# Kernel optimization log

Hardware: AMD Instinct MI355X
Metric: run time of the kernel (lower is better)

## Reference

```python
import jax, jax.numpy as jnp
import numpy as np
import math

B, C, H, W = 2, 256, 64, 64
E = 256           # embed_dim
AE = 64           # angle embed dim = embed_dim // 4
NH = 3            # num angle hypotheses
HEADS = 8
HALF = AE // 2    # 32 sin/cos frequencies

# 3x3 kernel tap grid (dy, dx), row-major, matching torchvision DeformConv2d tap order
KY = jnp.array([-1,-1,-1, 0,0,0, 1,1,1], jnp.float32)
KX = jnp.array([-1, 0, 1,-1,0,1,-1,0,1], jnp.float32)
# assumed angle hypothesis deltas around the predicted angle
HYPO_DELTAS = (-math.pi/12, 0.0, math.pi/12)


def conv2d(x, w, b, pad):
    y = jax.lax.conv_general_dilated(x, w, (1, 1), [(pad, pad), (pad, pad)],
                                     dimension_numbers=('NCHW', 'OIHW', 'NCHW'))
    return y + b[None, :, None, None]


def gen_offsets(angles):
    """Rotate the base 3x3 kernel taps by the per-pixel angle; offset = rotated - base.
    angles: (B, H*W, 1) -> offsets (B, 18, H, W), (dy,dx) interleaved per tap."""
    a = angles.reshape(-1, H, W)
    c = jnp.cos(a)[..., None]           # (B,H,W,1)
    s = jnp.sin(a)[..., None]
    ry = KX * s + KY * c                # rotated y of each tap, (B,H,W,9)
    rx = KX * c - KY * s                # rotated x
    off = jnp.stack([ry - KY, rx - KX], axis=-1)   # (B,H,W,9,2)
    return off.reshape(-1, H, W, 18).transpose(0, 3, 1, 2)


def deform_conv(x, offsets, w, b):
    """DeformConv2d k=3, stride=1, pad=1, dilation=1, zero padding outside.
    x (B,C,H,W), offsets (B,18,H,W), w (O,C,3,3)."""
    off = offsets.reshape(x.shape[0], 9, 2, H, W)
    oy = off[:, :, 0].transpose(0, 2, 3, 1)          # (B,H,W,9)
    ox = off[:, :, 1].transpose(0, 2, 3, 1)
    hh = jnp.arange(H, dtype=jnp.float32)[None, :, None, None]
    ww = jnp.arange(W, dtype=jnp.float32)[None, None, :, None]
    py = hh + KY + oy                                # sample y, (B,H,W,9)
    px = ww + KX + ox
    y0 = jnp.floor(py)
    x0 = jnp.floor(px)
    wy = (py - y0)[:, None]                          # (B,1,H,W,9)
    wx = (px - x0)[:, None]

    def gather(yi, xi):
        valid = (yi >= 0) & (yi <= H - 1) & (xi >= 0) & (xi <= W - 1)
        yc = jnp.clip(yi, 0, H - 1).astype(jnp.int32)
        xc = jnp.clip(xi, 0, W - 1).astype(jnp.int32)
        g = jax.vmap(lambda img, yy, xx: img[:, yy, xx])(x, yc, xc)  # (B,C,H,W,9)
        return g * valid[:, None].astype(x.dtype)

    samp = (gather(y0, x0) * (1 - wy) * (1 - wx)
            + gather(y0, x0 + 1) * (1 - wy) * wx
            + gather(y0 + 1, x0) * wy * (1 - wx)
            + gather(y0 + 1, x0 + 1) * wy * wx)      # (B,C,H,W,9)
    w9 = w.reshape(w.shape[0], w.shape[1], 9)
    return jnp.einsum('bchwk,ock->bohw', samp, w9) + b[None, :, None, None]


def angle_encode(angles, freq_mult, w1, b1, ln_g, ln_b, w2, b2):
    an = (angles / (math.pi / 2))[..., 0]                       # (B,HW) le90 norm
    dim_t = jnp.arange(HALF, dtype=jnp.float32) / HALF * math.pi
    ae = an[..., None] * (freq_mult * dim_t)                    # (B,HW,HALF)
    emb = jnp.concatenate([jnp.sin(ae), jnp.cos(ae)], axis=-1)  # (B,HW,AE)
    h = emb @ w1.T + b1
    mu = h.mean(-1, keepdims=True)
    var = h.var(-1, keepdims=True)
    h = (h - mu) * jax.lax.rsqrt(var + 1e-5) * ln_g + ln_b
    return jax.nn.relu(h) @ w2.T + b2


def mha(q, kv, in_w, in_b, out_w, out_b):
    # q (L,1,E), kv (L,NH,E); torch nn.MultiheadAttention math
    wq, wk, wv = jnp.split(in_w, 3, axis=0)
    bq, bk, bv = jnp.split(in_b, 3)
    hd = E // HEADS
    Q = (q @ wq.T + bq).reshape(-1, 1, HEADS, hd).transpose(0, 2, 1, 3)
    K = (kv @ wk.T + bk).reshape(-1, NH, HEADS, hd).transpose(0, 2, 1, 3)
    V = (kv @ wv.T + bv).reshape(-1, NH, HEADS, hd).transpose(0, 2, 1, 3)
    attn = jax.nn.softmax(jnp.einsum('lhqd,lhkd->lhqk', Q, K) / math.sqrt(hd), axis=-1)
    o = jnp.einsum('lhqk,lhkd->lhqd', attn, V).transpose(0, 2, 1, 3).reshape(-1, 1, E)
    return o @ out_w.T + out_b


def group_norm(x, g, b, groups=32, eps=1e-5):
    Bq, Cc, Hh, Ww = x.shape
    xg = x.reshape(Bq, groups, Cc // groups, Hh, Ww)
    mu = xg.mean((2, 3, 4), keepdims=True)
    var = xg.var((2, 3, 4), keepdims=True)
    xn = ((xg - mu) * jax.lax.rsqrt(var + eps)).reshape(x.shape)
    return xn * g[None, :, None, None] + b[None, :, None, None]


def setup_inputs() -> dict:
    key = jax.random.key(0)
    ks = iter(jax.random.split(key, 32))
    r = lambda *s: jax.random.normal(next(ks), s, jnp.float32) * 0.05
    z = lambda *s: jnp.zeros(s, jnp.float32)
    return {
        'features': jax.random.normal(next(ks), (B, C, H, W), jnp.float32),
        'ap_w1': r(C // 4, C, 3, 3), 'ap_b1': z(C // 4),
        'ap_w2': r(1, C // 4, 1, 1), 'ap_b2': z(1),
        'freq_mult': jnp.ones((HALF,), jnp.float32),
        'ae_w1': r(AE, AE), 'ae_b1': z(AE),
        'ae_ln_g': jnp.ones((AE,), jnp.float32), 'ae_ln_b': z(AE),
        'ae_w2': r(AE, AE), 'ae_b2': z(AE),
        'dc_w': r(E, C, 3, 3), 'dc_b': z(E),
        'attn_in_w': r(3 * E, E), 'attn_in_b': z(3 * E),
        'attn_out_w': r(E, E), 'attn_out_b': z(E),
        'ja_w1': r(E, E + AE, 1, 1), 'ja_b1': z(E),
        'ja_w2': r(E, E, 1, 1), 'ja_b2': z(E),
        'op_w1': r(E, E, 3, 3), 'op_b1': z(E),
        'gn_g': jnp.ones((E,), jnp.float32), 'gn_b': z(E),
        'op_w2': r(E, E, 1, 1), 'op_b2': z(E),
    }


def reference(features, ap_w1, ap_b1, ap_w2, ap_b2, freq_mult, ae_w1, ae_b1,
              ae_ln_g, ae_ln_b, ae_w2, ae_b2, dc_w, dc_b, attn_in_w, attn_in_b,
              attn_out_w, attn_out_b, ja_w1, ja_b1, ja_w2, ja_b2, op_w1, op_b1,
              gn_g, gn_b, op_w2, op_b2):
    # 1) angle prediction
    h1 = jax.nn.relu(conv2d(features, ap_w1, ap_b1, 1))
    angles = conv2d(h1, ap_w2, ap_b2, 0).reshape(B, H * W, 1)
    # 2) periodic angle encoding
    angle_embed = angle_encode(angles, freq_mult, ae_w1, ae_b1, ae_ln_g, ae_ln_b, ae_w2, ae_b2)
    # 3) rotation-aware deformable alignment
    aligned = deform_conv(features, gen_offsets(angles), dc_w, dc_b)
    # 4) multi-angle hypotheses fused by per-pixel attention
    cand = [deform_conv(features, gen_offsets(angles + d), dc_w, dc_b) for d in HYPO_DELTAS]
    feat_stack = jnp.stack(cand, axis=1)                       # (B,NH,E,H,W)
    q = aligned.transpose(0, 2, 3, 1).reshape(B * H * W, 1, E)
    kv = feat_stack.transpose(0, 3, 4, 1, 2).reshape(B * H * W, NH, E)
    fused = mha(q, kv, attn_in_w, attn_in_b, attn_out_w, attn_out_b)
    fused = fused.reshape(B, H, W, E).transpose(0, 3, 1, 2)
    # 5) joint angle-spatial attention gate
    ae_sp = angle_embed.reshape(B, H, W, AE).transpose(0, 3, 1, 2)
    ji = jnp.concatenate([fused, ae_sp], axis=1)
    gate = jax.nn.sigmoid(conv2d(jax.nn.relu(conv2d(ji, ja_w1, ja_b1, 0)), ja_w2, ja_b2, 0))
    enh = fused * gate + fused
    # 6) output projection
    o = jax.nn.relu(group_norm(conv2d(enh, op_w1, op_b1, 1), gn_g, gn_b))
    return conv2d(o, op_w2, op_b2, 0)
```

## Files before the change

kernel.cpp:

```cpp
#include <hip/hip_runtime.h>

#define PI_F 3.14159265358979323846f
#define HWSZ 4096
#define NPIX 8192

typedef __attribute__((ext_vector_type(8))) short short8;
typedef __attribute__((ext_vector_type(4))) short short4_t;
typedef __attribute__((ext_vector_type(4))) float f32x4;

__device__ __forceinline__ short f2bf(float x){
  unsigned u = __float_as_uint(x);
  unsigned r = (u + 0x7FFFu + ((u >> 16) & 1u)) >> 16;
  return (short)r;
}
__device__ __forceinline__ float bf2f(short v){
  return __uint_as_float(((unsigned)(unsigned short)v) << 16);
}

__device__ __forceinline__ float wsum64(float v){
  #pragma unroll
  for (int m = 32; m >= 1; m >>= 1) v += __shfl_xor(v, m, 64);
  return v;
}
__device__ __forceinline__ float wsum8(float v){
  v += __shfl_xor(v, 1, 64);
  v += __shfl_xor(v, 2, 64);
  v += __shfl_xor(v, 4, 64);
  return v;
}

__device__ __forceinline__ void gl_lds(const short* g, short* s){
  __builtin_amdgcn_global_load_lds(
      (const __attribute__((address_space(1))) unsigned int*)g,
      (__attribute__((address_space(3))) unsigned int*)s, 16, 0, 0);
}

__global__ void k_prepall(const float* __restrict__ dc_w, const float* __restrict__ op_w1,
    const float* __restrict__ ap_w1, const float* __restrict__ features,
    const float* __restrict__ s0, const float* __restrict__ s1,
    const float* __restrict__ s2, const float* __restrict__ s3, const float* __restrict__ s4,
    short* __restrict__ enh_pad, short* __restrict__ Bdc, short* __restrict__ B2op,
    short* __restrict__ B3, short* __restrict__ A3,
    short* __restrict__ d0, short* __restrict__ d1,
    short* __restrict__ d2, short* __restrict__ d3, short* __restrict__ d4){
  __shared__ short tile[2304];
  __shared__ float ft[32][33];
  int bx = blockIdx.x, tid = threadIdx.x;
  if (bx < 2178){
    int i = bx*256 + tid;
    if (i < 557568) ((short4_t*)enh_pad)[i] = (short4_t){0,0,0,0};
  } else if (bx < 2434){
    int o = bx - 2178;
    const float* wo = dc_w + (size_t)o*2304;
    for (int i = tid; i < 2304; i += 256){
      int c = i / 9, k = i - c*9;
      tile[k*256 + c] = f2bf(wo[i]);
    }
    __syncthreads();
    for (int i = tid; i < 2304; i += 256){
      int k = i >> 8, c = i & 255;
      Bdc[((size_t)(k*256 + o))*256 + c] = tile[i];
    }
  } else if (bx < 2690){
    int o = bx - 2434;
    const float* wo = op_w1 + (size_t)o*2304;
    for (int i = tid; i < 2304; i += 256){
      int c = i / 9, k = i - c*9;
      tile[k*256 + c] = f2bf(wo[i]);
    }
    __syncthreads();
    short* out = B2op + (size_t)o*2304;
    for (int i = tid; i < 2304; i += 256) out[i] = tile[i];
  } else if (bx < 3330){
    int n = bx - 2690, c = tid;
    short hi = 0;
    if (n < 576){
      int o = n & 63, k = n >> 6;
      hi = f2bf(ap_w1[((size_t)o*256 + c)*9 + k]);
    }
    B3[(size_t)n*512 + c] = hi;
    B3[(size_t)n*512 + 256 + c] = hi;
  } else if (bx < 5186){
    int i = (bx - 3330)*256 + tid;
    if (i < 196608) d0[i] = f2bf(s0[i]);
    else if (i < 262144) d1[i-196608] = f2bf(s1[i-196608]);
    else if (i < 344064) d2[i-262144] = f2bf(s2[i-262144]);
    else if (i < 409600) d3[i-344064] = f2bf(s3[i-344064]);
    else if (i < 475136) d4[i-409600] = f2bf(s4[i-409600]);
  } else {
    int bid = bx - 5186;
    int z = bid >> 10;
    int rem = bid & 1023;
    int p0 = (rem & 127)*32, c0 = (rem >> 7)*32;
    int tx = tid & 31, ty = tid >> 5;
    #pragma unroll
    for (int i = ty; i < 32; i += 8)
      ft[i][tx] = features[((size_t)z*256 + c0 + i)*HWSZ + p0 + tx];
    __syncthreads();
    #pragma unroll
    for (int i = ty; i < 32; i += 8){
      float x = ft[tx][i];
      short hi = f2bf(x);
      short lo = f2bf(x - bf2f(hi));
      size_t p = (size_t)z*HWSZ + p0 + i;
      A3[p*512 + c0 + tx] = hi;
      A3[p*512 + 256 + c0 + tx] = lo;
    }
  }
}

__global__ __launch_bounds__(256) void k_mainA(const short* __restrict__ A3,
    const short* __restrict__ Bdc, const short* __restrict__ B3,
    short* __restrict__ G, float* __restrict__ T){
  __shared__ alignas(16) short sA[2][128*32];
  __shared__ alignas(16) short sB[2][128*32];
  bool isG = blockIdx.y < 18;
  const short* B; int K, ldb, n0;
  if (isG){ B = Bdc; K = 256; ldb = 256; n0 = blockIdx.y*128; }
  else    { B = B3;  K = 512; ldb = 512; n0 = ((int)blockIdx.y - 18)*128; }
  int tid = threadIdx.x;
  int w = tid >> 6, l = tid & 63;
  int wc = w & 1, wr = w >> 1;
  int ml = l & 15, g = l >> 4;
  int srow = tid >> 2;
  int sch = (tid & 3)*8;
  int m0 = blockIdx.x*128;
  const short* Agp = A3 + (size_t)(m0 + srow)*512 + sch;
  const short* Bgp = B + (size_t)(n0 + srow)*ldb + sch;
  short* sAd = &sA[0][srow*32 + sch];
  short* sBd = &sB[0][srow*32 + sch];
  f32x4 acc[4][4];
  #pragma unroll
  for (int i = 0; i < 4; ++i)
    #pragma unroll
    for (int j = 0; j < 4; ++j) acc[i][j] = (f32x4){0.f,0.f,0.f,0.f};
  #define STG(bf, kt) { \
    gl_lds(Agp + (kt)*32, sAd + (bf)*4096); \
    gl_lds(Agp + (size_t)64*512 + (kt)*32, sAd + (bf)*4096 + 2048); \
    gl_lds(Bgp + (kt)*32, sBd + (bf)*4096); \
    gl_lds(Bgp + (size_t)64*ldb + (kt)*32, sBd + (bf)*4096 + 2048); \
  }
  int nk = K >> 5;
  STG(0, 0)
  int buf = 0;
  for (int kt = 0; kt < nk; ++kt){
    __syncthreads();
    if (kt + 1 < nk){ STG(buf^1, kt+1) }
    short8 af[4], bq[4];
    #pragma unroll
    for (int i = 0; i < 4; ++i)
      af[i] = *(const short8*)&sA[buf][(wr*64 + i*16 + ml)*32 + g*8];
    #pragma unroll
    for (int j = 0; j < 4; ++j)
      bq[j] = *(const short8*)&sB[buf][(wc*64 + j*16 + ml)*32 + g*8];
    #pragma unroll
    for (int i = 0; i < 4; ++i)
      #pragma unroll
      for (int j = 0; j < 4; ++j)
        acc[i][j] = __builtin_amdgcn_mfma_f32_16x16x32_bf16(af[i], bq[j], acc[i][j], 0, 0, 0);
    buf ^= 1;
  }
  #undef STG
  int m0w = m0 + wr*64;
  int n0w = n0 + wc*64;
  #pragma unroll
  for (int fm = 0; fm < 4; ++fm)
    #pragma unroll
    for (int fn = 0; fn < 4; ++fn)
      #pragma unroll
      for (int r = 0; r < 4; ++r){
        int row = m0w + fm*16 + g*4 + r;
        int col = n0w + fn*16 + ml;
        float v = acc[fm][fn][r];
        if (isG)
          G[(size_t)(col>>8)*2097152 + (size_t)row*256 + (col&255)] = f2bf(v);
        else
          T[(size_t)row*640 + col] = v;
      }
}

template<int EPI, int BM, int BN = 128>
__global__ __launch_bounds__(256) void k_gemml(const short* __restrict__ A,
    const short* __restrict__ B, void* __restrict__ Cv,
    const float* __restrict__ bias, const short* __restrict__ aux,
    int K, int ldc){
  constexpr int NWC = BN/64;
  constexpr int NWR = 4/NWC;
  constexpr int WM = BM/NWR;
  constexpr int AF = WM/16;
  __shared__ alignas(16) short sA[2][BM*32];
  __shared__ alignas(16) short sB[2][BN*32];
  int tid = threadIdx.x;
  int w = tid >> 6, l = tid & 63;
  int wc = w % NWC, wr = w / NWC;
  int ml = l & 15, g = l >> 4;
  int srow = tid >> 2;
  int sch = (tid & 3)*8;
  int m0 = blockIdx.x*BM, n0 = blockIdx.y*BN;
  const short* Agp = A + (size_t)(m0 + srow)*K + sch;
  const short* Bgp = B + (size_t)(n0 + srow)*K + sch;
  short* sAd = &sA[0][srow*32 + sch];
  short* sBd = &sB[0][srow*32 + sch];
  f32x4 acc[AF][4];
  #pragma unroll
  for (int i = 0; i < AF; ++i)
    #pragma unroll
    for (int j = 0; j < 4; ++j) acc[i][j] = (f32x4){0.f,0.f,0.f,0.f};

  #define STAGE(bf, kt) { \
    _Pragma("unroll") \
    for (int c = 0; c < BM/64; ++c) \
      gl_lds(Agp + (size_t)(c*64)*K + (kt)*32, sAd + (bf)*BM*32 + c*2048); \
    _Pragma("unroll") \
    for (int c = 0; c < BN/64; ++c) \
      gl_lds(Bgp + (size_t)(c*64)*K + (kt)*32, sBd + (bf)*BN*32 + c*2048); \
  }
  int nk = K >> 5;
  STAGE(0, 0)
  int buf = 0;
  for (int kt = 0; kt < nk; ++kt){
    __syncthreads();
    if (kt + 1 < nk){ STAGE(buf^1, kt+1) }
    short8 af[AF], bq[4];
    #pragma unroll
    for (int i = 0; i < AF; ++i)
      af[i] = *(const short8*)&sA[buf][(wr*WM + i*16 + ml)*32 + g*8];
    #pragma unroll
    for (int j = 0; j < 4; ++j)
      bq[j] = *(const short8*)&sB[buf][(wc*64 + j*16 + ml)*32 + g*8];
    #pragma unroll
    for (int i = 0; i < AF; ++i)
      #pragma unroll
      for (int j = 0; j < 4; ++j)
        acc[i][j] = __builtin_amdgcn_mfma_f32_16x16x32_bf16(af[i], bq[j], acc[i][j], 0, 0, 0);
    buf ^= 1;
  }
  #undef STAGE

  int m0w = m0 + wr*WM;
  int n0w = n0 + wc*64;
  #pragma unroll
  for (int fm = 0; fm < AF; ++fm)
    #pragma unroll
    for (int fn = 0; fn < 4; ++fn)
      #pragma unroll
      for (int r = 0; r < 4; ++r){
        int row = m0w + fm*16 + g*4 + r;
        int col = n0w + fn*16 + ml;
        float v = acc[fm][fn][r];
        if constexpr (EPI == 2){
          ((short*)Cv)[(size_t)row*ldc + col] = f2bf(fmaxf(v + bias[col], 0.f));
        } else if constexpr (EPI == 6){
          float f = bf2f(aux[(size_t)row*320 + col]);
          float s = 1.f/(1.f + __expf(-(v + bias[col])));
          int b = row >> 12, hw = row & 4095;
          int pi = b*4356 + ((hw>>6)+1)*66 + (hw&63) + 1;
          ((short*)Cv)[(size_t)pi*256 + col] = f2bf(f * (1.f + s));
        }
      }
}

__global__ __launch_bounds__(256) void k_qkv(const short* __restrict__ cand,
    const short* __restrict__ inw, const float* __restrict__ inb,
    short* __restrict__ KV, short* __restrict__ Qb){
  const short* A; const short* B; short* C; const float* bias; int ldc, m0, n0;
  if (blockIdx.y < 4){
    A = cand; B = inw + (size_t)256*256; C = KV; bias = inb + 256; ldc = 512;
    m0 = blockIdx.x*128; n0 = blockIdx.y*128;
  } else {
    if (blockIdx.x >= 128) return;
    A = cand + (size_t)NPIX*256; B = inw; C = Qb; bias = inb; ldc = 256;
    m0 = (blockIdx.x >> 1)*128; n0 = (blockIdx.x & 1)*128;
  }
  __shared__ alignas(16) short sA[2][128*32];
  __shared__ alignas(16) short sB[2][128*32];
  int tid = threadIdx.x;
  int w = tid >> 6, l = tid & 63;
  int wc = w & 1, wr = w >> 1;
  int ml = l & 15, g = l >> 4;
  int srow = tid >> 2;
  int sch = (tid & 3)*8;
  const short* Agp = A + (size_t)(m0 + srow)*256 + sch;
  const short* Bgp = B + (size_t)(n0 + srow)*256 + sch;
  short* sAd = &sA[0][srow*32 + sch];
  short* sBd = &sB[0][srow*32 + sch];
  f32x4 acc[4][4];
  #pragma unroll
  for (int i = 0; i < 4; ++i)
    #pragma unroll
    for (int j = 0; j < 4; ++j) acc[i][j] = (f32x4){0.f,0.f,0.f,0.f};
  #define STG2(bf, kt) { \
    gl_lds(Agp + (kt)*32, sAd + (bf)*4096); \
    gl_lds(Agp + (size_t)64*256 + (kt)*32, sAd + (bf)*4096 + 2048); \
    gl_lds(Bgp + (kt)*32, sBd + (bf)*4096); \
    gl_lds(Bgp + (size_t)64*256 + (kt)*32, sBd + (bf)*4096 + 2048); \
  }
  STG2(0, 0)
  int buf = 0;
  for (int kt = 0; kt < 8; ++kt){
    __syncthreads();
    if (kt + 1 < 8){ STG2(buf^1, kt+1) }
    short8 af[4], bq[4];
    #pragma unroll
    for (int i = 0; i < 4; ++i)
      af[i] = *(const short8*)&sA[buf][(wr*64 + i*16 + ml)*32 + g*8];
    #pragma unroll
    for (int j = 0; j < 4; ++j)
      bq[j] = *(const short8*)&sB[buf][(wc*64 + j*16 + ml)*32 + g*8];
    #pragma unroll
    for (int i = 0; i < 4; ++i)
      #pragma unroll
      for (int j = 0; j < 4; ++j)
        acc[i][j] = __builtin_amdgcn_mfma_f32_16x16x32_bf16(af[i], bq[j], acc[i][j], 0, 0, 0);
    buf ^= 1;
  }
  #undef STG2
  int m0w = m0 + wr*64;
  int n0w = n0 + wc*64;
  #pragma unroll
  for (int fm = 0; fm < 4; ++fm)
    #pragma unroll
    for (int fn = 0; fn < 4; ++fn)
      #pragma unroll
      for (int r = 0; r < 4; ++r){
        int row = m0w + fm*16 + g*4 + r;
        int col = n0w + fn*16 + ml;
        C[(size_t)row*ldc + col] = f2bf(acc[fm][fn][r] + bias[col]);
      }
}

__global__ __launch_bounds__(256) void k_attnproj(const short* __restrict__ Qb,
    const short* __restrict__ KVb, const short* __restrict__ wot,
    const float* __restrict__ outb, short* __restrict__ gateA){
  __shared__ alignas(16) short sO[64*256];
  __shared__ alignas(16) short sB[2][64*32];
  int tid = threadIdx.x;
  int m0 = blockIdx.x*64, n0 = blockIdx.y*64;
  int srow = tid >> 2, sch = (tid & 3)*8;
  const short* Bgp = wot + (size_t)(n0 + srow)*256 + sch;
  short* sBd = &sB[0][srow*32 + sch];
  gl_lds(Bgp, sBd);
  int lane = tid & 63;
  int sub = tid >> 6;
  const float sc = 0.17677669529663688f;
  #pragma unroll 2
  for (int it = 0; it < 16; ++it){
    int lp = it*4 + sub;
    int p = m0 + lp;
    float q[4];
    { short4_t t = *(const short4_t*)(Qb + (size_t)p*256 + lane*4);
      #pragma unroll
      for (int j = 0; j < 4; ++j) q[j] = bf2f(t[j]); }
    float kv[3][2][4];
    #pragma unroll
    for (int i = 0; i < 3; ++i){
      const short* rp = KVb + (size_t)(i*NPIX + p)*512 + lane*4;
      short4_t kt = *(const short4_t*)rp;
      short4_t vt = *(const short4_t*)(rp + 256);
      #pragma unroll
      for (int j = 0; j < 4; ++j){ kv[i][0][j] = bf2f(kt[j]); kv[i][1][j] = bf2f(vt[j]); }
    }
    float s[3];
    #pragma unroll
    for (int i = 0; i < 3; ++i){
      float d = 0.f;
      #pragma unroll
      for (int j = 0; j < 4; ++j) d = fmaf(q[j], kv[i][0][j], d);
      s[i] = wsum8(d) * sc;
    }
    float m = fmaxf(s[0], fmaxf(s[1], s[2]));
    float e0 = __expf(s[0]-m), e1 = __expf(s[1]-m), e2 = __expf(s[2]-m);
    float inv = 1.f/(e0+e1+e2);
    short4_t ot;
    #pragma unroll
    for (int j = 0; j < 4; ++j)
      ot[j] = f2bf((e0*kv[0][1][j] + e1*kv[1][1][j] + e2*kv[2][1][j]) * inv);
    *(short4_t*)&sO[lp*256 + lane*4] = ot;
  }
  int w = sub, ml = lane & 15, g = lane >> 4;
  f32x4 acc[4];
  #pragma unroll
  for (int j = 0; j < 4; ++j) acc[j] = (f32x4){0.f,0.f,0.f,0.f};
  int buf = 0;
  for (int kt = 0; kt < 8; ++kt){
    __syncthreads();
    if (kt + 1 < 8) gl_lds(Bgp + (kt+1)*32, sBd + (buf^1)*2048);
    short8 af = *(const short8*)&sO[(w*16 + ml)*256 + kt*32 + g*8];
    short8 bq[4];
    #pragma unroll
    for (int j = 0; j < 4; ++j)
      bq[j] = *(const short8*)&sB[buf][(j*16 + ml)*32 + g*8];
    #pragma unroll
    for (int j = 0; j < 4; ++j)
      acc[j] = __builtin_amdgcn_mfma_f32_16x16x32_bf16(af, bq[j], acc[j], 0, 0, 0);
    buf ^= 1;
  }
  int m0w = m0 + w*16;
  #pragma unroll
  for (int fn = 0; fn < 4; ++fn)
    #pragma unroll
    for (int r = 0; r < 4; ++r){
      int row = m0w + g*4 + r;
      int col = n0 + fn*16 + ml;
      gateA[(size_t)row*320 + col] = f2bf(acc[fn][r] + outb[col]);
    }
}

__global__ __launch_bounds__(256) void k_igconv(const short* __restrict__ Xpad,
    const short* __restrict__ B2, float* __restrict__ PG){
  __shared__ alignas(16) short sA[2][64*32];
  __shared__ alignas(16) short sB[2][128*32];
  int zg = blockIdx.z;
  int tid = threadIdx.x;
  int w = tid >> 6, l = tid & 63;
  int wr = w & 1, wc = w >> 1;
  int ml = l & 15, g = l >> 4;
  int srow = tid >> 2;
  int sch = (tid & 3)*8;
  int m0 = blockIdx.x*64, n0 = blockIdx.y*128;
  int b = blockIdx.x >> 6, imgrow = blockIdx.x & 63;
  int qbase = b*4356 + (imgrow+1)*66 + srow + 1;
  const short* Bgp = B2 + (size_t)(n0 + srow)*2304 + zg*768 + sch;
  short* sAd = &sA[0][srow*32 + sch];
  short* sBd = &sB[0][srow*32 + sch];
  int toff[3];
  #pragma unroll
  for (int i = 0; i < 3; ++i){
    int t = zg*3 + i;
    toff[i] = (t/3 - 1)*66 + (t%3) - 1;
  }
  f32x4 acc[2][4];
  #pragma unroll
  for (int i = 0; i < 2; ++i)
    #pragma unroll
    for (int j = 0; j < 4; ++j) acc[i][j] = (f32x4){0.f,0.f,0.f,0.f};

  #define STG(bf, kt) { \
    int tap = (kt) >> 3, cofs = ((kt) & 7)*32; \
    gl_lds(Xpad + (size_t)(qbase + toff[tap])*256 + cofs + sch, sAd + (bf)*2048); \
    gl_lds(Bgp + (kt)*32, sBd + (bf)*4096); \
    gl_lds(Bgp + (size_t)64*2304 + (kt)*32, sBd + (bf)*4096 + 2048); \
  }
  STG(0, 0)
  int buf = 0;
  for (int kt = 0; kt < 24; ++kt){
    __syncthreads();
    if (kt < 23){ STG(buf^1, kt+1) }
    short8 af[2], bq[4];
    #pragma unroll
    for (int i = 0; i < 2; ++i)
      af[i] = *(const short8*)&sA[buf][(wr*32 + i*16 + ml)*32 + g*8];
    #pragma unroll
    for (int j = 0; j < 4; ++j)
      bq[j] = *(const short8*)&sB[buf][(wc*64 + j*16 + ml)*32 + g*8];
    #pragma unroll
    for (int i = 0; i < 2; ++i)
      #pragma unroll
      for (int j = 0; j < 4; ++j)
        acc[i][j] = __builtin_amdgcn_mfma_f32_16x16x32_bf16(af[i], bq[j], acc[i][j], 0, 0, 0);
    buf ^= 1;
  }
  #undef STG

  float* out = PG + (size_t)zg*2097152;
  int m0w = m0 + wr*32;
  int n0w = n0 + wc*64;
  #pragma unroll
  for (int fm = 0; fm < 2; ++fm)
    #pragma unroll
    for (int fn = 0; fn < 4; ++fn)
      #pragma unroll
      for (int r = 0; r < 4; ++r){
        int row = m0w + fm*16 + g*4 + r;
        int col = n0w + fn*16 + ml;
        out[(size_t)row*256 + col] = acc[fm][fn][r];
      }
}

__global__ void k_aph1enc(const float* __restrict__ T, const float* __restrict__ b1,
    const float* __restrict__ w2, const float* __restrict__ b2,
    const float* __restrict__ freq,
    const float* __restrict__ ew1, const float* __restrict__ eb1,
    const float* __restrict__ lng, const float* __restrict__ lnb,
    const float* __restrict__ ew2, const float* __restrict__ eb2,
    short* __restrict__ gateA, int2* __restrict__ moff, float4* __restrict__ mw){
  const int KYi[9] = {-1,-1,-1,0,0,0,1,1,1};
  const int KXi[9] = {-1,0,1,-1,0,1,-1,0,1};
  __shared__ float sang[4];
  int lane = threadIdx.x & 63;
  int wid = threadIdx.x >> 6;
  int p = blockIdx.x*4 + wid;
  int hw = p & 4095;
  int h = hw >> 6, w = hw & 63;
  float acc = b1[lane];
  #pragma unroll
  for (int k = 0; k < 9; ++k){
    int y = h + KYi[k], x = w + KXi[k];
    if (y < 0 || y > 63 || x < 0 || x > 63) continue;
    acc += T[(size_t)(p + KYi[k]*64 + KXi[k])*640 + k*64 + lane];
  }
  float av = wsum64(fmaxf(acc, 0.f) * w2[lane]) + b2[0];
  if (lane == 0) sang[wid] = av;
  float an = av * (2.0f / PI_F);
  int f = lane & 31;
  float ph = an * freq[f] * ((float)f * (PI_F / 32.0f));
  float emb = (lane < 32) ? __sinf(ph) : __cosf(ph);
  float hh = eb1[lane];
  const float* w1r = ew1 + lane*64;
  #pragma unroll 8
  for (int i = 0; i < 64; ++i){
    float e = __shfl(emb, i, 64);
    hh = fmaf(e, w1r[i], hh);
  }
  float mu = wsum64(hh) * (1.0f/64.0f);
  float d = hh - mu;
  float var = wsum64(d*d) * (1.0f/64.0f);
  float hn = fmaf(d * rsqrtf(var + 1e-5f), lng[lane], lnb[lane]);
  float r = fmaxf(hn, 0.f);
  float o = eb2[lane];
  const float* w2r = ew2 + lane*64;
  #pragma unroll 8
  for (int i = 0; i < 64; ++i){
    float e = __shfl(r, i, 64);
    o = fmaf(e, w2r[i], o);
  }
  gateA[(size_t)p*320 + 256 + lane] = f2bf(o);
  __syncthreads();
  int tid = threadIdx.x;
  if (tid < 108){
    int lp = tid / 27;
    int j = tid - lp*27;
    int pp = blockIdx.x*4 + lp;
    int hyp = j / 9;
    int tap = j - hyp*9;
    float ky = (float)(tap/3 - 1), kx = (float)(tap - (tap/3)*3 - 1);
    float a = sang[lp] + ((float)hyp - 1.0f) * (PI_F / 12.0f);
    float sn = __sinf(a), cs = __cosf(a);
    int b2i = pp >> 12, hw2 = pp & 4095;
    float py = (float)(hw2 >> 6) + kx*sn + ky*cs;
    float px = (float)(hw2 & 63) + kx*cs - ky*sn;
    float y0f = floorf(py), x0f = floorf(px);
    float wy = py - y0f, wx = px - x0f;
    int y0 = (int)y0f, x0 = (int)x0f;
    bool vx0 = (unsigned)x0 < 64u, vx1 = (unsigned)(x0+1) < 64u;
    bool vy0 = (unsigned)y0 < 64u, vy1 = (unsigned)(y0+1) < 64u;
    int xb = vx0 ? x0 : (vx1 ? x0+1 : 0);
    float sx0 = vx0 ? 1.f-wx : (vx1 ? wx : 0.f);
    float sx1 = (vx0 && vx1) ? wx : 0.f;
    int ry0 = vy0 ? y0 : 0;
    int ry1 = vy1 ? y0+1 : 0;
    float vw0 = vy0 ? 1.f-wy : 0.f;
    float vw1 = vy1 ? wy : 0.f;
    int base = (b2i << 12);
    int mi = pp*27 + j;
    moff[mi] = make_int2(tap*4194304 + (base + ry0*64 + xb)*512,
                         tap*4194304 + (base + ry1*64 + xb)*512);
    mw[mi] = make_float4(vw0*sx0, vw0*sx1, vw1*sx0, vw1*sx1);
  }
}

__global__ __launch_bounds__(256, 4) void k_sample(const short* __restrict__ G,
    const int2* __restrict__ moff, const float4* __restrict__ mw,
    const float* __restrict__ bias, short* __restrict__ cand){
  __shared__ int2 smo[216];
  __shared__ float4 smw[216];
  int id = blockIdx.x;
  int sw = (id & 7)*128 + (id >> 3);
  int tid = threadIdx.x;
  int pbase = sw*8;
  if (tid < 216){
    smo[tid] = moff[pbase*27 + tid];
    smw[tid] = mw[pbase*27 + tid];
  }
  __syncthreads();
  int lp = (tid >> 6)*2 + ((tid >> 5) & 1);
  int p = pbase + lp;
  int c8 = (tid & 31)*8;
  float av[3][8];
  {
    float4 b0 = *(const float4*)(bias + c8);
    float4 b1 = *(const float4*)(bias + c8 + 4);
    #pragma unroll
    for (int h2 = 0; h2 < 3; ++h2){
      av[h2][0]=b0.x; av[h2][1]=b0.y; av[h2][2]=b0.z; av[h2][3]=b0.w;
      av[h2][4]=b1.x; av[h2][5]=b1.y; av[h2][6]=b1.z; av[h2][7]=b1.w;
    }
  }
  #pragma unroll
  for (int hyp = 0; hyp < 3; ++hyp){
    #pragma unroll 3
    for (int tap = 0; tap < 9; ++tap){
      int idx = lp*27 + hyp*9 + tap;
      int2 o = smo[idx];
      float4 wv = smw[idx];
      const short* r0 = (const short*)((const char*)G + o.x) + c8;
      const short* r1 = (const short*)((const char*)G + o.y) + c8;
      short8 v00 = *(const short8*)r0;
      short8 v01 = *(const short8*)(r0 + 256);
      short8 v10 = *(const short8*)r1;
      short8 v11 = *(const short8*)(r1 + 256);
      #pragma unroll
      for (int e = 0; e < 8; ++e){
        float s = wv.x*bf2f(v00[e]) + wv.y*bf2f(v01[e]);
        s += wv.z*bf2f(v10[e]) + wv.w*bf2f(v11[e]);
        av[hyp][e] += s;
      }
    }
  }
  #pragma unroll
  for (int hyp = 0; hyp < 3; ++hyp){
    short8 o;
    #pragma unroll
    for (int e = 0; e < 8; ++e) o[e] = f2bf(av[hyp][e]);
    *(short8*)(cand + ((size_t)hyp*NPIX + p)*256 + c8) = o;
  }
}

__global__ void k_sum3stat(const float* __restrict__ PG, const float* __restrict__ bias,
    float* __restrict__ t, float* __restrict__ spart){
  int p0 = blockIdx.x * 8;
  int c = threadIdx.x;
  float bb = bias[c];
  float s = 0.f, s2 = 0.f;
  #pragma unroll
  for (int pp = 0; pp < 8; ++pp){
    size_t idx = (size_t)(p0+pp)*256 + c;
    float v = PG[idx] + PG[idx + 2097152] + PG[idx + 4194304] + bb;
    t[idx] = v;
    s += v; s2 = fmaf(v, v, s2);
  }
  s  += __shfl_xor(s, 1, 64);  s  += __shfl_xor(s, 2, 64);  s  += __shfl_xor(s, 4, 64);
  s2 += __shfl_xor(s2, 1, 64); s2 += __shfl_xor(s2, 2, 64); s2 += __shfl_xor(s2, 4, 64);
  if ((c & 7) == 0){
    int b = p0 >> 12;
    int bg = b*32 + (c >> 3);
    int blk = blockIdx.x & 511;
    spart[(size_t)(bg*512 + blk)*2]     = s;
    spart[(size_t)(bg*512 + blk)*2 + 1] = s2;
  }
}

__global__ void k_gnfin(const float* __restrict__ spart, float* __restrict__ stat){
  int bg = blockIdx.x;
  const float* sp = spart + (size_t)bg*1024;
  float s = 0.f, s2 = 0.f;
  for (int i = threadIdx.x; i < 512; i += 256){
    s += sp[i*2]; s2 += sp[i*2+1];
  }
  s = wsum64(s); s2 = wsum64(s2);
  __shared__ float rs[4], rs2[4];
  int wid = threadIdx.x >> 6;
  if ((threadIdx.x & 63) == 0){ rs[wid] = s; rs2[wid] = s2; }
  __syncthreads();
  if (threadIdx.x == 0){
    float S = rs[0]+rs[1]+rs[2]+rs[3];
    float S2 = rs2[0]+rs2[1]+rs2[2]+rs2[3];
    float mean = S * (1.f/32768.f);
    float var = S2 * (1.f/32768.f) - mean*mean;
    stat[bg*2]   = mean;
    stat[bg*2+1] = rsqrtf(var + 1e-5f);
  }
}

__global__ __launch_bounds__(256) void k_gnproj(const float* __restrict__ t,
    const float* __restrict__ stat, const float* __restrict__ gng,
    const float* __restrict__ gnb, const short* __restrict__ w2,
    const float* __restrict__ b2, float* __restrict__ out){
  __shared__ float cst[64*132];
  __shared__ alignas(16) short sB[2][128*32];
  short* sA = (short*)cst;
  int tid = threadIdx.x;
  int m0 = blockIdx.x*64;
  int b = m0 >> 12;
  int srow = tid >> 2, sch = (tid & 3)*8;
  const short* Bgp = w2 + (size_t)(blockIdx.y*128 + srow)*256 + sch;
  short* sBd = &sB[0][srow*32 + sch];
  gl_lds(Bgp, sBd);
  gl_lds(Bgp + (size_t)64*256, sBd + 2048);
  #pragma unroll 4
  for (int it = 0; it < 16; ++it){
    int c = it*256 + tid;
    int row = c >> 6;
    int col = (c & 63)*4;
    int g4 = col >> 3;
    float mean = stat[(b*32+g4)*2], rstd = stat[(b*32+g4)*2+1];
    float4 v = *(const float4*)(t + (size_t)(m0+row)*256 + col);
    float4 gg = *(const float4*)(gng + col);
    float4 bbv = *(const float4*)(gnb + col);
    short4_t o;
    o[0] = f2bf(fmaxf((v.x - mean)*rstd*gg.x + bbv.x, 0.f));
    o[1] = f2bf(fmaxf((v.y - mean)*rstd*gg.y + bbv.y, 0.f));
    o[2] = f2bf(fmaxf((v.z - mean)*rstd*gg.z + bbv.z, 0.f));
    o[3] = f2bf(fmaxf((v.w - mean)*rstd*gg.w + bbv.w, 0.f));
    *(short4_t*)&sA[row*256 + col] = o;
  }
  int w = tid >> 6, l = tid & 63;
  int wr = w & 1, wc = w >> 1;
  int ml = l & 15, g = l >> 4;
  f32x4 acc[2][4];
  #pragma unroll
  for (int i = 0; i < 2; ++i)
    #pragma unroll
    for (int j = 0; j < 4; ++j) acc[i][j] = (f32x4){0.f,0.f,0.f,0.f};
  int buf = 0;
  for (int kt = 0; kt < 8; ++kt){
    __syncthreads();
    if (kt + 1 < 8){
      gl_lds(Bgp + (kt+1)*32, sBd + (buf^1)*4096);
      gl_lds(Bgp + (size_t)64*256 + (kt+1)*32, sBd + (buf^1)*4096 + 2048);
    }
    short8 af[2], bq[4];
    #pragma unroll
    for (int i = 0; i < 2; ++i)
      af[i] = *(const short8*)&sA[(wr*32 + i*16 + ml)*256 + kt*32 + g*8];
    #pragma unroll
    for (int j = 0; j < 4; ++j)
      bq[j] = *(const short8*)&sB[buf][(wc*64 + j*16 + ml)*32 + g*8];
    #pragma unroll
    for (int i = 0; i < 2; ++i)
      #pragma unroll
      for (int j = 0; j < 4; ++j)
        acc[i][j] = __builtin_amdgcn_mfma_f32_16x16x32_bf16(af[i], bq[j], acc[i][j], 0, 0, 0);
    buf ^= 1;
  }
  __syncthreads();
  #pragma unroll
  for (int fm = 0; fm < 2; ++fm)
    #pragma unroll
    for (int fn = 0; fn < 4; ++fn)
      #pragma unroll
      for (int r = 0; r < 4; ++r){
        int cl = wc*64 + fn*16 + ml;
        cst[(wr*32 + fm*16 + g*4 + r)*132 + cl] = acc[fm][fn][r] + b2[blockIdx.y*128 + cl];
      }
  __syncthreads();
  int hw0 = m0 & 4095;
  int o = tid >> 1, seg = (tid & 1)*32;
  float* op = out + (((size_t)(b*256 + blockIdx.y*128 + o)) << 12) + hw0 + seg;
  #pragma unroll
  for (int i = 0; i < 32; i += 4){
    float4 vv = {cst[(seg+i)*132+o], cst[(seg+i+1)*132+o],
                 cst[(seg+i+2)*132+o], cst[(seg+i+3)*132+o]};
    *(float4*)(op + i) = vv;
  }
}

extern "C" void kernel_launch(void* const* d_in, const int* in_sizes, int n_in,
                              void* d_out, int out_size, void* d_ws, size_t ws_size,
                              hipStream_t stream){
  (void)in_sizes; (void)n_in; (void)out_size; (void)ws_size;
  const float* features   = (const float*)d_in[0];
  const float* ap_w1      = (const float*)d_in[1];
  const float* ap_b1      = (const float*)d_in[2];
  const float* ap_w2      = (const float*)d_in[3];
  const float* ap_b2      = (const float*)d_in[4];
  const float* freq       = (const float*)d_in[5];
  const float* ae_w1      = (const float*)d_in[6];
  const float* ae_b1      = (const float*)d_in[7];
  const float* ae_ln_g    = (const float*)d_in[8];
  const float* ae_ln_b    = (const float*)d_in[9];
  const float* ae_w2      = (const float*)d_in[10];
  const float* ae_b2      = (const float*)d_in[11];
  const float* dc_w       = (const float*)d_in[12];
  const float* dc_b       = (const float*)d_in[13];
  const float* attn_in_w  = (const float*)d_in[14];
  const float* attn_in_b  = (const float*)d_in[15];
  const float* attn_out_w = (const float*)d_in[16];
  const float* attn_out_b = (const float*)d_in[17];
  const float* ja_w1      = (const float*)d_in[18];
  const float* ja_b1      = (const float*)d_in[19];
  const float* ja_w2      = (const float*)d_in[20];
  const float* ja_b2      = (const float*)d_in[21];
  const float* op_w1      = (const float*)d_in[22];
  const float* op_b1      = (const float*)d_in[23];
  const float* gn_g       = (const float*)d_in[24];
  const float* gn_b       = (const float*)d_in[25];
  const float* op_w2      = (const float*)d_in[26];
  const float* op_b2      = (const float*)d_in[27];

  char* base = (char*)d_ws;
  #define ALLOC(ty, name, elems) ty* name = (ty*)base; base += (size_t)(elems)*sizeof(ty);
  ALLOC(short, Bdc,     2304*256)
  ALLOC(short, B2op,    256*2304)
  ALLOC(short, B3ap,    640*512)
  ALLOC(short, inw_bf,  768*256)
  ALLOC(short, wot_bf,  256*256)
  ALLOC(short, jw1_bf,  256*320)
  ALLOC(short, jw2_bf,  256*256)
  ALLOC(short, wop2_bf, 256*256)
  ALLOC(short, A3,      8192*512)
  ALLOC(short, Gbuf,    24576*768)
  ALLOC(short, gguard,  64)
  ALLOC(float, T_ap,    8192*640)
  ALLOC(short, cand_bf, 3*8192*256)
  ALLOC(short, gateA,   8192*320)
  ALLOC(short, hid_bf,  8192*256)
  ALLOC(short, enh_pad, 2*4356*256)
  ALLOC(float, tbuf,    8192*256)
  ALLOC(float, gstat,   128)
  ALLOC(float, spart,   65536)
  ALLOC(int,   moffb,   2*NPIX*27)
  ALLOC(float, mwb,     4*NPIX*27)
  #undef ALLOC
  (void)gguard;
  short* KVbuf = Gbuf;
  short* Qbuf  = Gbuf + (size_t)24576*512;
  float* PG    = (float*)Gbuf;
  int2*  moff  = (int2*)moffb;
  float4* mwv  = (float4*)mwb;

  k_prepall<<<7234, 256, 0, stream>>>(dc_w, op_w1, ap_w1, features,
      attn_in_w, attn_out_w, ja_w1, ja_w2, op_w2,
      enh_pad, Bdc, B2op, B3ap, A3,
      inw_bf, wot_bf, jw1_bf, jw2_bf, wop2_bf);

  k_mainA<<<dim3(64,23), 256, 0, stream>>>(A3, Bdc, B3ap, Gbuf, T_ap);
  k_aph1enc<<<2048, 256, 0, stream>>>(T_ap, ap_b1, ap_w2, ap_b2, freq,
                                      ae_w1, ae_b1, ae_ln_g, ae_ln_b, ae_w2, ae_b2,
                                      gateA, moff, mwv);
  k_sample<<<1024, 256, 0, stream>>>(Gbuf, moff, mwv, dc_b, cand_bf);
  k_qkv<<<dim3(192,5), 256, 0, stream>>>(cand_bf, inw_bf, attn_in_b, KVbuf, Qbuf);
  k_attnproj<<<dim3(128,4), 256, 0, stream>>>(Qbuf, KVbuf, wot_bf, attn_out_b, gateA);
  k_gemml<2,64,64><<<dim3(128,4), 256, 0, stream>>>(gateA, jw1_bf, hid_bf, ja_b1, nullptr, 320, 256);
  k_gemml<6,64,64><<<dim3(128,4), 256, 0, stream>>>(hid_bf, jw2_bf, enh_pad, ja_b2, gateA, 256, 256);
  k_igconv<<<dim3(128,2,3), 256, 0, stream>>>(enh_pad, B2op, PG);
  k_sum3stat<<<1024, 256, 0, stream>>>(PG, op_b1, tbuf, spart);
  k_gnfin<<<64, 256, 0, stream>>>(spart, gstat);
  k_gnproj<<<dim3(128,2), 256, 0, stream>>>(tbuf, gstat, gn_g, gn_b, wop2_bf, op_b2,
                                            (float*)d_out);
}
```

Measured before the change: 186.1 us.

## Zero only padding border, split igconv K into two chunks, widen cast blocks

```diff
diff --git a/kernel.cpp b/kernel.cpp
--- a/kernel.cpp
+++ b/kernel.cpp
@@ -46,11 +46,22 @@
   __shared__ short tile[2304];
   __shared__ float ft[32][33];
   int bx = blockIdx.x, tid = threadIdx.x;
-  if (bx < 2178){
+  if (bx < 130){
     int i = bx*256 + tid;
-    if (i < 557568) ((short4_t*)enh_pad)[i] = (short4_t){0,0,0,0};
-  } else if (bx < 2434){
-    int o = bx - 2178;
+    if (i < 33280){
+      int px = i >> 6;
+      int c4 = (i & 63) * 4;
+      int b = px >= 260 ? 1 : 0;
+      int r = px - b*260;
+      int row, col;
+      if (r < 66){ row = 0; col = r; }
+      else if (r < 132){ row = 65; col = r - 66; }
+      else { int rr = r - 132; row = (rr >> 1) + 1; col = (rr & 1)*65; }
+      int pp = b*4356 + row*66 + col;
+      *(short4_t*)(enh_pad + (size_t)pp*256 + c4) = (short4_t){0,0,0,0};
+    }
+  } else if (bx < 386){
+    int o = bx - 130;
     const float* wo = dc_w + (size_t)o*2304;
     for (int i = tid; i < 2304; i += 256){
       int c = i / 9, k = i - c*9;
@@ -61,8 +72,8 @@
       int k = i >> 8, c = i & 255;
       Bdc[((size_t)(k*256 + o))*256 + c] = tile[i];
     }
-  } else if (bx < 2690){
-    int o = bx - 2434;
+  } else if (bx < 642){
+    int o = bx - 386;
     const float* wo = op_w1 + (size_t)o*2304;
     for (int i = tid; i < 2304; i += 256){
       int c = i / 9, k = i - c*9;
@@ -71,8 +82,8 @@
     __syncthreads();
     short* out = B2op + (size_t)o*2304;
     for (int i = tid; i < 2304; i += 256) out[i] = tile[i];
-  } else if (bx < 3330){
-    int n = bx - 2690, c = tid;
+  } else if (bx < 1282){
+    int n = bx - 642, c = tid;
     short hi = 0;
     if (n < 576){
       int o = n & 63, k = n >> 6;
@@ -80,15 +91,19 @@
     }
     B3[(size_t)n*512 + c] = hi;
     B3[(size_t)n*512 + 256 + c] = hi;
-  } else if (bx < 5186){
-    int i = (bx - 3330)*256 + tid;
-    if (i < 196608) d0[i] = f2bf(s0[i]);
-    else if (i < 262144) d1[i-196608] = f2bf(s1[i-196608]);
-    else if (i < 344064) d2[i-262144] = f2bf(s2[i-262144]);
-    else if (i < 409600) d3[i-344064] = f2bf(s3[i-344064]);
-    else if (i < 475136) d4[i-409600] = f2bf(s4[i-409600]);
+  } else if (bx < 2210){
+    int i = (bx - 1282)*512 + tid;
+    #pragma unroll
+    for (int rep = 0; rep < 2; ++rep){
+      if (i < 196608) d0[i] = f2bf(s0[i]);
+      else if (i < 262144) d1[i-196608] = f2bf(s1[i-196608]);
+      else if (i < 344064) d2[i-262144] = f2bf(s2[i-262144]);
+      else if (i < 409600) d3[i-344064] = f2bf(s3[i-344064]);
+      else if (i < 475136) d4[i-409600] = f2bf(s4[i-409600]);
+      i += 256;
+    }
   } else {
-    int bid = bx - 5186;
+    int bid = bx - 2210;
     int z = bid >> 10;
     int rem = bid & 1023;
     int p0 = (rem & 127)*32, c0 = (rem >> 7)*32;
@@ -411,6 +426,8 @@
   __shared__ alignas(16) short sA[2][64*32];
   __shared__ alignas(16) short sB[2][128*32];
   int zg = blockIdx.z;
+  int tapb = zg ? 5 : 0;
+  int nk = zg ? 32 : 40;
   int tid = threadIdx.x;
   int w = tid >> 6, l = tid & 63;
   int wr = w & 1, wc = w >> 1;
@@ -420,14 +437,15 @@
   int m0 = blockIdx.x*64, n0 = blockIdx.y*128;
   int b = blockIdx.x >> 6, imgrow = blockIdx.x & 63;
   int qbase = b*4356 + (imgrow+1)*66 + srow + 1;
-  const short* Bgp = B2 + (size_t)(n0 + srow)*2304 + zg*768 + sch;
+  const short* Bgp = B2 + (size_t)(n0 + srow)*2304 + tapb*256 + sch;
   short* sAd = &sA[0][srow*32 + sch];
   short* sBd = &sB[0][srow*32 + sch];
-  int toff[3];
-  #pragma unroll
-  for (int i = 0; i < 3; ++i){
-    int t = zg*3 + i;
-    toff[i] = (t/3 - 1)*66 + (t%3) - 1;
+  int toff[5];
+  #pragma unroll
+  for (int i = 0; i < 5; ++i){
+    int t = tapb + i;
+    if (t < 9) toff[i] = (t/3 - 1)*66 + (t%3) - 1;
+    else toff[i] = 0;
   }
   f32x4 acc[2][4];
   #pragma unroll
@@ -443,9 +461,9 @@
   }
   STG(0, 0)
   int buf = 0;
-  for (int kt = 0; kt < 24; ++kt){
+  for (int kt = 0; kt < nk; ++kt){
     __syncthreads();
-    if (kt < 23){ STG(buf^1, kt+1) }
+    if (kt < nk - 1){ STG(buf^1, kt+1) }
     short8 af[2], bq[4];
     #pragma unroll
     for (int i = 0; i < 2; ++i)
@@ -625,7 +643,7 @@
   #pragma unroll
   for (int pp = 0; pp < 8; ++pp){
     size_t idx = (size_t)(p0+pp)*256 + c;
-    float v = PG[idx] + PG[idx + 2097152] + PG[idx + 4194304] + bb;
+    float v = PG[idx] + PG[idx + 2097152] + bb;
     t[idx] = v;
     s += v; s2 = fmaf(v, v, s2);
   }
@@ -790,7 +808,7 @@
   ALLOC(short, wop2_bf, 256*256)
   ALLOC(short, A3,      8192*512)
   ALLOC(short, Gbuf,    24576*768)
-  ALLOC(short, gguard,  64)
+  ALLOC(short, gguard,  256)
   ALLOC(float, T_ap,    8192*640)
   ALLOC(short, cand_bf, 3*8192*256)
   ALLOC(short, gateA,   8192*320)
@@ -809,7 +827,7 @@
   int2*  moff  = (int2*)moffb;
   float4* mwv  = (float4*)mwb;
 
-  k_prepall<<<7234, 256, 0, stream>>>(dc_w, op_w1, ap_w1, features,
+  k_prepall<<<4258, 256, 0, stream>>>(dc_w, op_w1, ap_w1, features,
       attn_in_w, attn_out_w, ja_w1, ja_w2, op_w2,
       enh_pad, Bdc, B2op, B3ap, A3,
       inw_bf, wot_bf, jw1_bf, jw2_bf, wop2_bf);
@@ -823,7 +841,7 @@
   k_attnproj<<<dim3(128,4), 256, 0, stream>>>(Qbuf, KVbuf, wot_bf, attn_out_b, gateA);
   k_gemml<2,64,64><<<dim3(128,4), 256, 0, stream>>>(gateA, jw1_bf, hid_bf, ja_b1, nullptr, 320, 256);
   k_gemml<6,64,64><<<dim3(128,4), 256, 0, stream>>>(hid_bf, jw2_bf, enh_pad, ja_b2, gateA, 256, 256);
-  k_igconv<<<dim3(128,2,3), 256, 0, stream>>>(enh_pad, B2op, PG);
+  k_igconv<<<dim3(128,2,2), 256, 0, stream>>>(enh_pad, B2op, PG);
   k_sum3stat<<<1024, 256, 0, stream>>>(PG, op_b1, tbuf, spart);
   k_gnfin<<<64, 256, 0, stream>>>(spart, gstat);
   k_gnproj<<<dim3(128,2), 256, 0, stream>>>(tbuf, gstat, gn_g, gn_b, wop2_bf, op_b2,
```

Measured after the change: 188.1 us. Within noise of the previous version (+1.1%).
